# Kernel tuning notes

Measured on AMD Instinct MI355X. Metric: run time of the kernel, lower is better.

## Reference

```python
import jax, jax.numpy as jnp
import numpy as np

N = 100000
E = 1600000
IN_FEATS = 128
OUT_FEATS = 64


def setup_inputs() -> dict:
    key = jax.random.key(0)
    ks = jax.random.split(key, 8)
    node_feat = jax.random.normal(ks[0], (N, IN_FEATS), dtype=jnp.float32)
    edge_feat = jax.random.normal(ks[1], (E, 1), dtype=jnp.float32)
    # Linear params (PyTorch Linear: y = x @ W^T + b; we store W already transposed as [in, out])
    W_node = jax.random.normal(ks[2], (IN_FEATS, OUT_FEATS), dtype=jnp.float32) / np.sqrt(IN_FEATS)
    b_node = jax.random.normal(ks[3], (OUT_FEATS,), dtype=jnp.float32) * 0.01
    W_edge = jax.random.normal(ks[4], (1, OUT_FEATS), dtype=jnp.float32)
    b_edge = jax.random.normal(ks[5], (OUT_FEATS,), dtype=jnp.float32) * 0.01
    src = jax.random.randint(ks[6], (E,), 0, N, dtype=jnp.int32)
    dst = jax.random.randint(ks[7], (E,), 0, N, dtype=jnp.int32)
    return {"node_feat": node_feat, "edge_feat": edge_feat, "W_node": W_node,
            "b_node": b_node, "W_edge": W_edge, "b_edge": b_edge,
            "src": src, "dst": dst}


def reference(node_feat, edge_feat, W_node, b_node, W_edge, b_edge, src, dst):
    n_nodes = node_feat.shape[0]
    # node linear: h = node_fc(node_feat)  -> [N, out]
    h = node_feat @ W_node + b_node
    # edge linear: he = edge_fc(edge_feat) -> [E, out]
    he = edge_feat @ W_edge + b_edge
    # u_add_e: m = h[src] + he  (gather + add)  -> [E, out]
    m = h[src] + he
    # mean aggregate over destination nodes (segment mean; 0 for isolated nodes, as in DGL)
    msg_sum = jax.ops.segment_sum(m, dst, num_segments=n_nodes)  # [N, out]
    deg = jax.ops.segment_sum(jnp.ones((dst.shape[0],), dtype=m.dtype), dst, num_segments=n_nodes)  # [N]
    h_new = msg_sum / jnp.maximum(deg, 1.0)[:, None]
    return h_new
```

## Files before the change

### kernel.cpp

```cpp
#include <hip/hip_runtime.h>

#define IN_F 128
#define OUT_F 64
#define BSH 7
#define BNODES 128
#define NBMAX 800
#define MSC 4096
#define CAPB 4096

typedef __attribute__((ext_vector_type(8))) short short8;
typedef __attribute__((ext_vector_type(4))) float f32x4;

static __device__ __forceinline__ unsigned short f2bf(float f) {
    unsigned u = __float_as_uint(f);
    u += 0x7FFF + ((u >> 16) & 1);
    return (unsigned short)(u >> 16);
}

__global__ void prep(const float* __restrict__ W, unsigned short* __restrict__ Wt,
                     int* __restrict__ gcur, int nb) {
    int i = blockIdx.x * 256 + threadIdx.x;
    if (i < OUT_F * IN_F) {
        int o = i >> 7, k = i & 127;
        Wt[i] = f2bf(W[k * OUT_F + o]);
    }
    if (i < nb) gcur[i] = i * CAPB;
}

__global__ __launch_bounds__(256) void node_linear_mfma(const float* __restrict__ nf,
                                                        const unsigned short* __restrict__ Wt,
                                                        const float* __restrict__ bn,
                                                        unsigned short* __restrict__ h16,
                                                        int n_nodes, int n_tiles) {
    const int lane = threadIdx.x & 63;
    const int wid  = threadIdx.x >> 6;
    const int l15  = lane & 15;
    const int kq   = lane >> 4;

    short8 bfrag[4][4];
#pragma unroll
    for (int c = 0; c < 4; ++c)
#pragma unroll
        for (int ks = 0; ks < 4; ++ks)
            bfrag[c][ks] = *(const short8*)&Wt[(c * 16 + l15) * IN_F + ks * 32 + kq * 8];

    float bv[4];
#pragma unroll
    for (int c = 0; c < 4; ++c) bv[c] = bn[c * 16 + l15];

    for (int tile = blockIdx.x * 4 + wid; tile < n_tiles; tile += gridDim.x * 4) {
        int arow = tile * 16 + l15;
        if (arow >= n_nodes) arow = n_nodes - 1;
        const float* rp = nf + (size_t)arow * IN_F + kq * 8;

        f32x4 acc[4];
#pragma unroll
        for (int c = 0; c < 4; ++c) acc[c] = (f32x4){bv[c], bv[c], bv[c], bv[c]};

#pragma unroll
        for (int ks = 0; ks < 4; ++ks) {
            float4 x0 = *(const float4*)(rp + ks * 32);
            float4 x1 = *(const float4*)(rp + ks * 32 + 4);
            short8 af;
            af[0] = (short)f2bf(x0.x); af[1] = (short)f2bf(x0.y);
            af[2] = (short)f2bf(x0.z); af[3] = (short)f2bf(x0.w);
            af[4] = (short)f2bf(x1.x); af[5] = (short)f2bf(x1.y);
            af[6] = (short)f2bf(x1.z); af[7] = (short)f2bf(x1.w);
#pragma unroll
            for (int c = 0; c < 4; ++c)
                acc[c] = __builtin_amdgcn_mfma_f32_16x16x32_bf16(af, bfrag[c][ks], acc[c], 0, 0, 0);
        }

#pragma unroll
        for (int j = 0; j < 4; ++j) {
            int node = tile * 16 + kq * 4 + j;
            if (node < n_nodes) {
#pragma unroll
                for (int c = 0; c < 4; ++c)
                    h16[(size_t)node * OUT_F + c * 16 + l15] = f2bf(acc[c][j]);
            }
        }
    }
}

__global__ __launch_bounds__(1024) void multisplit(const int* __restrict__ src,
                                                   const int* __restrict__ dst,
                                                   const float* __restrict__ ef,
                                                   int* __restrict__ gcur,
                                                   int2* __restrict__ es,
                                                   int n_edges, int nb) {
    __shared__ int2 stage[MSC];
    __shared__ unsigned short sbuck[MSC];
    __shared__ int lhist[NBMAX];
    __shared__ int lcur[NBMAX];
    __shared__ int gbase[NBMAX];
    __shared__ int wtot[16];

    const int t = threadIdx.x;
    const int cb = blockIdx.x * MSC;
    const int valid = min(MSC, n_edges - cb);
    if (valid <= 0) return;

    for (int i = t; i < nb; i += 1024) lhist[i] = 0;

    int dr[4]; int sr[4]; float fr[4];
#pragma unroll
    for (int k = 0; k < 4; ++k) {
        int i = t + (k << 10);
        if (i < valid) { dr[k] = dst[cb + i]; sr[k] = src[cb + i]; fr[k] = ef[cb + i]; }
        else           { dr[k] = -1; sr[k] = 0; fr[k] = 0.f; }
    }
    __syncthreads();

#pragma unroll
    for (int k = 0; k < 4; ++k)
        if (dr[k] >= 0) atomicAdd(&lhist[dr[k] >> BSH], 1);
    __syncthreads();

    const int wv = t >> 6, lane = t & 63;
    int v = (t < nb) ? lhist[t] : 0;
    int sc = v;
#pragma unroll
    for (int off = 1; off < 64; off <<= 1) {
        int x = __shfl_up(sc, off, 64);
        if (lane >= off) sc += x;
    }
    if (lane == 63) wtot[wv] = sc;
    __syncthreads();
    if (t < 16) {
        int w = wtot[t];
        int s2 = w;
#pragma unroll
        for (int off = 1; off < 16; off <<= 1) {
            int x = __shfl_up(s2, off, 64);
            if (t >= off) s2 += x;
        }
        wtot[t] = s2 - w;
    }
    __syncthreads();
    if (t < nb) lcur[t] = wtot[wv] + (sc - v);
    __syncthreads();

    for (int b = t; b < nb; b += 1024) {
        int c = lhist[b];
        gbase[b] = c ? atomicAdd(&gcur[b], c) : 0;
    }
#pragma unroll
    for (int k = 0; k < 4; ++k) {
        if (dr[k] >= 0) {
            int b = dr[k] >> BSH;
            int p = atomicAdd(&lcur[b], 1);
            int dl = dr[k] & (BNODES - 1);
            stage[p] = make_int2((dl << 17) | sr[k], __float_as_int(fr[k]));
            sbuck[p] = (unsigned short)b;
        }
    }
    __syncthreads();

    for (int i = t; i < valid; i += 1024) {
        int b = sbuck[i];
        int pos = gbase[b] + (i - (lcur[b] - lhist[b]));
        if (pos < (b + 1) * CAPB) es[pos] = stage[i];
    }
}

__global__ __launch_bounds__(512, 8) void aggregate(const unsigned short* __restrict__ h16,
                                                    const int2* __restrict__ es,
                                                    const int* __restrict__ gcur,
                                                    const float* __restrict__ We,
                                                    const float* __restrict__ be,
                                                    float* __restrict__ out, int n_nodes) {
    __shared__ int2 stage[CAPB];
    __shared__ int lhist8[8][BNODES];
    __shared__ int lhist[BNODES];
    __shared__ int lbase[BNODES];
    __shared__ int lcur[BNODES];

    const int t = threadIdx.x;
    const int bkt = blockIdx.x;
    const int s0 = bkt * CAPB;
    int cnt = gcur[bkt] - s0;
    if (cnt > CAPB) cnt = CAPB;

    ((int*)lhist8)[t] = 0;
    ((int*)lhist8)[t + 512] = 0;
    __syncthreads();

    const int wv = t >> 6;
    int2 er[8];
#pragma unroll
    for (int k = 0; k < 8; ++k) {
        int i = t + (k << 9);
        if (i < cnt) er[k] = es[s0 + i];
    }
#pragma unroll
    for (int k = 0; k < 8; ++k) {
        int i = t + (k << 9);
        if (i < cnt) atomicAdd(&lhist8[wv][((unsigned)er[k].x) >> 17], 1);
    }
    __syncthreads();

    if (t < 64) {
        int a = 0, b = 0;
#pragma unroll
        for (int w = 0; w < 8; ++w) { a += lhist8[w][t << 1]; b += lhist8[w][(t << 1) + 1]; }
        lhist[t << 1] = a; lhist[(t << 1) + 1] = b;
        int s = a + b;
#pragma unroll
        for (int off = 1; off < 64; off <<= 1) {
            int x = __shfl_up(s, off, 64);
            if (t >= off) s += x;
        }
        int excl = s - (a + b);
        lbase[t << 1] = excl;       lcur[t << 1] = excl;
        lbase[(t << 1) + 1] = excl + a; lcur[(t << 1) + 1] = excl + a;
    }
    __syncthreads();

#pragma unroll
    for (int k = 0; k < 8; ++k) {
        int i = t + (k << 9);
        if (i < cnt) {
            int b = ((unsigned)er[k].x) >> 17;
            int p = atomicAdd(&lcur[b], 1);
            stage[p] = er[k];
        }
    }
    __syncthreads();

    const int lane = t & 63;
    const int q    = lane >> 4;
    const int o4e  = (lane & 15) << 2;
    const float4 we4 = *(const float4*)&We[o4e];
    const float4 be4 = *(const float4*)&be[o4e];

#pragma unroll
    for (int p = 0; p < 8; ++p) {
        const int dlA = (wv << 4) + (p << 1);
        const int dlB = dlA + 1;
        const int jA = lbase[dlA], dgA = lhist[dlA];
        const int jB = lbase[dlB], dgB = lhist[dlB];
        float4 aA = make_float4(0.f, 0.f, 0.f, 0.f);
        float4 aB = make_float4(0.f, 0.f, 0.f, 0.f);
        float sxA = 0.f, sxB = 0.f;
        const int jm = dgA > dgB ? dgA : dgB;
        for (int j = 0; j < jm; j += 4) {
            int2 eA = make_int2(0, 0), eB = make_int2(0, 0);
            if (j + q < dgA) eA = stage[jA + j + q];
            if (j + q < dgB) eB = stage[jB + j + q];
            uint2 hA = make_uint2(0u, 0u), hB = make_uint2(0u, 0u);
            if (j + q < dgA) hA = *(const uint2*)&h16[((size_t)(eA.x & 0x1FFFF) << 6) + o4e];
            if (j + q < dgB) hB = *(const uint2*)&h16[((size_t)(eB.x & 0x1FFFF) << 6) + o4e];
            aA.x += __uint_as_float(hA.x << 16);
            aA.y += __uint_as_float(hA.x & 0xFFFF0000u);
            aA.z += __uint_as_float(hA.y << 16);
            aA.w += __uint_as_float(hA.y & 0xFFFF0000u);
            sxA  += __int_as_float(eA.y);
            aB.x += __uint_as_float(hB.x << 16);
            aB.y += __uint_as_float(hB.x & 0xFFFF0000u);
            aB.z += __uint_as_float(hB.y << 16);
            aB.w += __uint_as_float(hB.y & 0xFFFF0000u);
            sxB  += __int_as_float(eB.y);
        }
#define RED_(v) { v += __shfl_xor(v, 16, 64); v += __shfl_xor(v, 32, 64); }
        RED_(aA.x) RED_(aA.y) RED_(aA.z) RED_(aA.w) RED_(sxA)
        RED_(aB.x) RED_(aB.y) RED_(aB.z) RED_(aB.w) RED_(sxB)
#undef RED_
        if (q == 0) {
            int nodeA = (bkt << BSH) + dlA;
            if (nodeA < n_nodes) {
                float4 r = make_float4(0.f, 0.f, 0.f, 0.f);
                if (dgA > 0) {
                    float dgf = (float)dgA, inv = 1.f / dgf;
                    r.x = (aA.x + we4.x * sxA + dgf * be4.x) * inv;
                    r.y = (aA.y + we4.y * sxA + dgf * be4.y) * inv;
                    r.z = (aA.z + we4.z * sxA + dgf * be4.z) * inv;
                    r.w = (aA.w + we4.w * sxA + dgf * be4.w) * inv;
                }
                *(float4*)&out[((size_t)nodeA << 6) + o4e] = r;
            }
            int nodeB = (bkt << BSH) + dlB;
            if (nodeB < n_nodes) {
                float4 r = make_float4(0.f, 0.f, 0.f, 0.f);
                if (dgB > 0) {
                    float dgf = (float)dgB, inv = 1.f / dgf;
                    r.x = (aB.x + we4.x * sxB + dgf * be4.x) * inv;
                    r.y = (aB.y + we4.y * sxB + dgf * be4.y) * inv;
                    r.z = (aB.z + we4.z * sxB + dgf * be4.z) * inv;
                    r.w = (aB.w + we4.w * sxB + dgf * be4.w) * inv;
                }
                *(float4*)&out[((size_t)nodeB << 6) + o4e] = r;
            }
        }
    }
}

extern "C" void kernel_launch(void* const* d_in, const int* in_sizes, int n_in,
                              void* d_out, int out_size, void* d_ws, size_t ws_size,
                              hipStream_t stream) {
    const float* nf  = (const float*)d_in[0];
    const float* ef  = (const float*)d_in[1];
    const float* Wn  = (const float*)d_in[2];
    const float* bn  = (const float*)d_in[3];
    const float* We  = (const float*)d_in[4];
    const float* be  = (const float*)d_in[5];
    const int*   src = (const int*)d_in[6];
    const int*   dst = (const int*)d_in[7];
    float* out = (float*)d_out;

    const int n_nodes = in_sizes[0] / IN_F;
    const int n_edges = in_sizes[6];
    const int nb = (n_nodes + BNODES - 1) >> BSH;
    const int n_tiles = (n_nodes + 15) / 16;

    char* w = (char*)d_ws;
    unsigned short* h16 = (unsigned short*)w; w += (size_t)n_nodes * OUT_F * sizeof(unsigned short);
    int2* es  = (int2*)w; w += (size_t)nb * CAPB * sizeof(int2);
    int* gcur = (int*)w;  w += (size_t)NBMAX * sizeof(int);
    unsigned short* Wt = (unsigned short*)w; w += (size_t)OUT_F * IN_F * sizeof(unsigned short);

    prep<<<32, 256, 0, stream>>>(Wn, Wt, gcur, nb);
    node_linear_mfma<<<782, 256, 0, stream>>>(nf, Wt, bn, h16, n_nodes, n_tiles);
    multisplit<<<(n_edges + MSC - 1) / MSC, 1024, 0, stream>>>(src, dst, ef, gcur, es, n_edges, nb);
    aggregate<<<nb, 512, 0, stream>>>(h16, es, gcur, We, be, out, n_nodes);
}
```

Measured before the change: 82.42 us.

## Pack bucket counters, enlarge multisplit chunks, widen aggregate gathers, one tile per wave

The multisplit kernel now handles 6144 edges per block instead of 4096. It packs two bucket cursors into one 32-bit atomic, which halves the global atomics and precomputes the scatter base offsets. Aggregate gathers 16-byte bf16 rows with 8 lanes per edge instead of 8-byte rows with 16 lanes, and relaxes its occupancy hint. The node linear kernel launches one tile per wave instead of grid-striding. Risks are 16-bit counter overflow if a bucket exceeds 65535 edges, higher register pressure, and more LDS per multisplit block.

```diff
diff --git a/kernel.cpp b/kernel.cpp
--- a/kernel.cpp
+++ b/kernel.cpp
@@ -5,7 +5,7 @@
 #define BSH 7
 #define BNODES 128
 #define NBMAX 800
-#define MSC 4096
+#define MSC 6144
 #define CAPB 4096
 
 typedef __attribute__((ext_vector_type(8))) short short8;
@@ -18,13 +18,13 @@
 }
 
 __global__ void prep(const float* __restrict__ W, unsigned short* __restrict__ Wt,
-                     int* __restrict__ gcur, int nb) {
+                     unsigned* __restrict__ gcur2, int npair) {
     int i = blockIdx.x * 256 + threadIdx.x;
     if (i < OUT_F * IN_F) {
         int o = i >> 7, k = i & 127;
         Wt[i] = f2bf(W[k * OUT_F + o]);
     }
-    if (i < nb) gcur[i] = i * CAPB;
+    if (i < npair) gcur2[i] = 0u;
 }
 
 __global__ __launch_bounds__(256) void node_linear_mfma(const float* __restrict__ nf,
@@ -36,6 +36,8 @@
     const int wid  = threadIdx.x >> 6;
     const int l15  = lane & 15;
     const int kq   = lane >> 4;
+    const int tile = blockIdx.x * 4 + wid;
+    if (tile >= n_tiles) return;
 
     short8 bfrag[4][4];
 #pragma unroll
@@ -48,37 +50,35 @@
 #pragma unroll
     for (int c = 0; c < 4; ++c) bv[c] = bn[c * 16 + l15];
 
-    for (int tile = blockIdx.x * 4 + wid; tile < n_tiles; tile += gridDim.x * 4) {
-        int arow = tile * 16 + l15;
-        if (arow >= n_nodes) arow = n_nodes - 1;
-        const float* rp = nf + (size_t)arow * IN_F + kq * 8;
-
-        f32x4 acc[4];
-#pragma unroll
-        for (int c = 0; c < 4; ++c) acc[c] = (f32x4){bv[c], bv[c], bv[c], bv[c]};
-
-#pragma unroll
-        for (int ks = 0; ks < 4; ++ks) {
-            float4 x0 = *(const float4*)(rp + ks * 32);
-            float4 x1 = *(const float4*)(rp + ks * 32 + 4);
-            short8 af;
-            af[0] = (short)f2bf(x0.x); af[1] = (short)f2bf(x0.y);
-            af[2] = (short)f2bf(x0.z); af[3] = (short)f2bf(x0.w);
-            af[4] = (short)f2bf(x1.x); af[5] = (short)f2bf(x1.y);
-            af[6] = (short)f2bf(x1.z); af[7] = (short)f2bf(x1.w);
+    int arow = tile * 16 + l15;
+    if (arow >= n_nodes) arow = n_nodes - 1;
+    const float* rp = nf + (size_t)arow * IN_F + kq * 8;
+
+    f32x4 acc[4];
+#pragma unroll
+    for (int c = 0; c < 4; ++c) acc[c] = (f32x4){bv[c], bv[c], bv[c], bv[c]};
+
+#pragma unroll
+    for (int ks = 0; ks < 4; ++ks) {
+        float4 x0 = *(const float4*)(rp + ks * 32);
+        float4 x1 = *(const float4*)(rp + ks * 32 + 4);
+        short8 af;
+        af[0] = (short)f2bf(x0.x); af[1] = (short)f2bf(x0.y);
+        af[2] = (short)f2bf(x0.z); af[3] = (short)f2bf(x0.w);
+        af[4] = (short)f2bf(x1.x); af[5] = (short)f2bf(x1.y);
+        af[6] = (short)f2bf(x1.z); af[7] = (short)f2bf(x1.w);
+#pragma unroll
+        for (int c = 0; c < 4; ++c)
+            acc[c] = __builtin_amdgcn_mfma_f32_16x16x32_bf16(af, bfrag[c][ks], acc[c], 0, 0, 0);
+    }
+
+#pragma unroll
+    for (int j = 0; j < 4; ++j) {
+        int node = tile * 16 + kq * 4 + j;
+        if (node < n_nodes) {
 #pragma unroll
             for (int c = 0; c < 4; ++c)
-                acc[c] = __builtin_amdgcn_mfma_f32_16x16x32_bf16(af, bfrag[c][ks], acc[c], 0, 0, 0);
-        }
-
-#pragma unroll
-        for (int j = 0; j < 4; ++j) {
-            int node = tile * 16 + kq * 4 + j;
-            if (node < n_nodes) {
-#pragma unroll
-                for (int c = 0; c < 4; ++c)
-                    h16[(size_t)node * OUT_F + c * 16 + l15] = f2bf(acc[c][j]);
-            }
+                h16[(size_t)node * OUT_F + c * 16 + l15] = f2bf(acc[c][j]);
         }
     }
 }
@@ -86,7 +86,7 @@
 __global__ __launch_bounds__(1024) void multisplit(const int* __restrict__ src,
                                                    const int* __restrict__ dst,
                                                    const float* __restrict__ ef,
-                                                   int* __restrict__ gcur,
+                                                   unsigned* __restrict__ gcur2,
                                                    int2* __restrict__ es,
                                                    int n_edges, int nb) {
     __shared__ int2 stage[MSC];
@@ -103,9 +103,9 @@
 
     for (int i = t; i < nb; i += 1024) lhist[i] = 0;
 
-    int dr[4]; int sr[4]; float fr[4];
-#pragma unroll
-    for (int k = 0; k < 4; ++k) {
+    int dr[6]; int sr[6]; float fr[6];
+#pragma unroll
+    for (int k = 0; k < 6; ++k) {
         int i = t + (k << 10);
         if (i < valid) { dr[k] = dst[cb + i]; sr[k] = src[cb + i]; fr[k] = ef[cb + i]; }
         else           { dr[k] = -1; sr[k] = 0; fr[k] = 0.f; }
@@ -113,7 +113,7 @@
     __syncthreads();
 
 #pragma unroll
-    for (int k = 0; k < 4; ++k)
+    for (int k = 0; k < 6; ++k)
         if (dr[k] >= 0) atomicAdd(&lhist[dr[k] >> BSH], 1);
     __syncthreads();
 
@@ -141,12 +141,23 @@
     if (t < nb) lcur[t] = wtot[wv] + (sc - v);
     __syncthreads();
 
-    for (int b = t; b < nb; b += 1024) {
-        int c = lhist[b];
-        gbase[b] = c ? atomicAdd(&gcur[b], c) : 0;
-    }
-#pragma unroll
-    for (int k = 0; k < 4; ++k) {
+    for (int i2 = t; i2 < (nb >> 1); i2 += 1024) {
+        int b0 = i2 << 1;
+        int c0 = lhist[b0], c1 = lhist[b0 + 1];
+        unsigned ret = 0u;
+        if (c0 | c1) ret = atomicAdd(&gcur2[i2], (unsigned)c0 | ((unsigned)c1 << 16));
+        gbase[b0]     = b0 * CAPB + (int)(ret & 0xFFFFu);
+        gbase[b0 + 1] = (b0 + 1) * CAPB + (int)(ret >> 16);
+    }
+    if ((nb & 1) && t == 0) {
+        int b0 = nb - 1;
+        int c0 = lhist[b0];
+        unsigned ret = 0u;
+        if (c0) ret = atomicAdd(&gcur2[nb >> 1], (unsigned)c0);
+        gbase[b0] = b0 * CAPB + (int)(ret & 0xFFFFu);
+    }
+#pragma unroll
+    for (int k = 0; k < 6; ++k) {
         if (dr[k] >= 0) {
             int b = dr[k] >> BSH;
             int p = atomicAdd(&lcur[b], 1);
@@ -157,16 +168,19 @@
     }
     __syncthreads();
 
+    for (int b = t; b < nb; b += 1024) gbase[b] -= (lcur[b] - lhist[b]);
+    __syncthreads();
+
     for (int i = t; i < valid; i += 1024) {
         int b = sbuck[i];
-        int pos = gbase[b] + (i - (lcur[b] - lhist[b]));
+        int pos = gbase[b] + i;
         if (pos < (b + 1) * CAPB) es[pos] = stage[i];
     }
 }
 
-__global__ __launch_bounds__(512, 8) void aggregate(const unsigned short* __restrict__ h16,
+__global__ __launch_bounds__(512, 6) void aggregate(const unsigned short* __restrict__ h16,
                                                     const int2* __restrict__ es,
-                                                    const int* __restrict__ gcur,
+                                                    const unsigned* __restrict__ gcur2,
                                                     const float* __restrict__ We,
                                                     const float* __restrict__ be,
                                                     float* __restrict__ out, int n_nodes) {
@@ -179,7 +193,8 @@
     const int t = threadIdx.x;
     const int bkt = blockIdx.x;
     const int s0 = bkt * CAPB;
-    int cnt = gcur[bkt] - s0;
+    unsigned packed = gcur2[bkt >> 1];
+    int cnt = (bkt & 1) ? (int)(packed >> 16) : (int)(packed & 0xFFFFu);
     if (cnt > CAPB) cnt = CAPB;
 
     ((int*)lhist8)[t] = 0;
@@ -212,7 +227,7 @@
             if (t >= off) s += x;
         }
         int excl = s - (a + b);
-        lbase[t << 1] = excl;       lcur[t << 1] = excl;
+        lbase[t << 1] = excl;           lcur[t << 1] = excl;
         lbase[(t << 1) + 1] = excl + a; lcur[(t << 1) + 1] = excl + a;
     }
     __syncthreads();
@@ -229,67 +244,81 @@
     __syncthreads();
 
     const int lane = t & 63;
-    const int q    = lane >> 4;
-    const int o4e  = (lane & 15) << 2;
-    const float4 we4 = *(const float4*)&We[o4e];
-    const float4 be4 = *(const float4*)&be[o4e];
-
-#pragma unroll
+    const int q    = lane >> 3;
+    const int o8   = (lane & 7) << 3;
+    const float4 weL = *(const float4*)&We[o8];
+    const float4 weH = *(const float4*)&We[o8 + 4];
+    const float4 beL = *(const float4*)&be[o8];
+    const float4 beH = *(const float4*)&be[o8 + 4];
+
     for (int p = 0; p < 8; ++p) {
         const int dlA = (wv << 4) + (p << 1);
         const int dlB = dlA + 1;
         const int jA = lbase[dlA], dgA = lhist[dlA];
         const int jB = lbase[dlB], dgB = lhist[dlB];
-        float4 aA = make_float4(0.f, 0.f, 0.f, 0.f);
-        float4 aB = make_float4(0.f, 0.f, 0.f, 0.f);
+        float aA[8] = {0.f,0.f,0.f,0.f,0.f,0.f,0.f,0.f};
+        float aB[8] = {0.f,0.f,0.f,0.f,0.f,0.f,0.f,0.f};
         float sxA = 0.f, sxB = 0.f;
         const int jm = dgA > dgB ? dgA : dgB;
-        for (int j = 0; j < jm; j += 4) {
+        for (int j = 0; j < jm; j += 8) {
             int2 eA = make_int2(0, 0), eB = make_int2(0, 0);
             if (j + q < dgA) eA = stage[jA + j + q];
             if (j + q < dgB) eB = stage[jB + j + q];
-            uint2 hA = make_uint2(0u, 0u), hB = make_uint2(0u, 0u);
-            if (j + q < dgA) hA = *(const uint2*)&h16[((size_t)(eA.x & 0x1FFFF) << 6) + o4e];
-            if (j + q < dgB) hB = *(const uint2*)&h16[((size_t)(eB.x & 0x1FFFF) << 6) + o4e];
-            aA.x += __uint_as_float(hA.x << 16);
-            aA.y += __uint_as_float(hA.x & 0xFFFF0000u);
-            aA.z += __uint_as_float(hA.y << 16);
-            aA.w += __uint_as_float(hA.y & 0xFFFF0000u);
-            sxA  += __int_as_float(eA.y);
-            aB.x += __uint_as_float(hB.x << 16);
-            aB.y += __uint_as_float(hB.x & 0xFFFF0000u);
-            aB.z += __uint_as_float(hB.y << 16);
-            aB.w += __uint_as_float(hB.y & 0xFFFF0000u);
-            sxB  += __int_as_float(eB.y);
-        }
-#define RED_(v) { v += __shfl_xor(v, 16, 64); v += __shfl_xor(v, 32, 64); }
-        RED_(aA.x) RED_(aA.y) RED_(aA.z) RED_(aA.w) RED_(sxA)
-        RED_(aB.x) RED_(aB.y) RED_(aB.z) RED_(aB.w) RED_(sxB)
+            uint4 hA = make_uint4(0u,0u,0u,0u), hB = make_uint4(0u,0u,0u,0u);
+            if (j + q < dgA) hA = *(const uint4*)&h16[((size_t)(eA.x & 0x1FFFF) << 6) + o8];
+            if (j + q < dgB) hB = *(const uint4*)&h16[((size_t)(eB.x & 0x1FFFF) << 6) + o8];
+            aA[0] += __uint_as_float(hA.x << 16); aA[1] += __uint_as_float(hA.x & 0xFFFF0000u);
+            aA[2] += __uint_as_float(hA.y << 16); aA[3] += __uint_as_float(hA.y & 0xFFFF0000u);
+            aA[4] += __uint_as_float(hA.z << 16); aA[5] += __uint_as_float(hA.z & 0xFFFF0000u);
+            aA[6] += __uint_as_float(hA.w << 16); aA[7] += __uint_as_float(hA.w & 0xFFFF0000u);
+            sxA   += __int_as_float(eA.y);
+            aB[0] += __uint_as_float(hB.x << 16); aB[1] += __uint_as_float(hB.x & 0xFFFF0000u);
+            aB[2] += __uint_as_float(hB.y << 16); aB[3] += __uint_as_float(hB.y & 0xFFFF0000u);
+            aB[4] += __uint_as_float(hB.z << 16); aB[5] += __uint_as_float(hB.z & 0xFFFF0000u);
+            aB[6] += __uint_as_float(hB.w << 16); aB[7] += __uint_as_float(hB.w & 0xFFFF0000u);
+            sxB   += __int_as_float(eB.y);
+        }
+#define RED_(v) { v += __shfl_xor(v, 8, 64); v += __shfl_xor(v, 16, 64); v += __shfl_xor(v, 32, 64); }
+#pragma unroll
+        for (int u = 0; u < 8; ++u) { RED_(aA[u]) }
+#pragma unroll
+        for (int u = 0; u < 8; ++u) { RED_(aB[u]) }
+        RED_(sxA) RED_(sxB)
 #undef RED_
         if (q == 0) {
             int nodeA = (bkt << BSH) + dlA;
             if (nodeA < n_nodes) {
-                float4 r = make_float4(0.f, 0.f, 0.f, 0.f);
+                float4 r0 = make_float4(0.f,0.f,0.f,0.f), r1 = r0;
                 if (dgA > 0) {
                     float dgf = (float)dgA, inv = 1.f / dgf;
-                    r.x = (aA.x + we4.x * sxA + dgf * be4.x) * inv;
-                    r.y = (aA.y + we4.y * sxA + dgf * be4.y) * inv;
-                    r.z = (aA.z + we4.z * sxA + dgf * be4.z) * inv;
-                    r.w = (aA.w + we4.w * sxA + dgf * be4.w) * inv;
+                    r0.x = (aA[0] + weL.x * sxA + dgf * beL.x) * inv;
+                    r0.y = (aA[1] + weL.y * sxA + dgf * beL.y) * inv;
+                    r0.z = (aA[2] + weL.z * sxA + dgf * beL.z) * inv;
+                    r0.w = (aA[3] + weL.w * sxA + dgf * beL.w) * inv;
+                    r1.x = (aA[4] + weH.x * sxA + dgf * beH.x) * inv;
+                    r1.y = (aA[5] + weH.y * sxA + dgf * beH.y) * inv;
+                    r1.z = (aA[6] + weH.z * sxA + dgf * beH.z) * inv;
+                    r1.w = (aA[7] + weH.w * sxA + dgf * beH.w) * inv;
                 }
-                *(float4*)&out[((size_t)nodeA << 6) + o4e] = r;
+                *(float4*)&out[((size_t)nodeA << 6) + o8] = r0;
+                *(float4*)&out[((size_t)nodeA << 6) + o8 + 4] = r1;
             }
             int nodeB = (bkt << BSH) + dlB;
             if (nodeB < n_nodes) {
-                float4 r = make_float4(0.f, 0.f, 0.f, 0.f);
+                float4 r0 = make_float4(0.f,0.f,0.f,0.f), r1 = r0;
                 if (dgB > 0) {
                     float dgf = (float)dgB, inv = 1.f / dgf;
-                    r.x = (aB.x + we4.x * sxB + dgf * be4.x) * inv;
-                    r.y = (aB.y + we4.y * sxB + dgf * be4.y) * inv;
-                    r.z = (aB.z + we4.z * sxB + dgf * be4.z) * inv;
-                    r.w = (aB.w + we4.w * sxB + dgf * be4.w) * inv;
+                    r0.x = (aB[0] + weL.x * sxB + dgf * beL.x) * inv;
+                    r0.y = (aB[1] + weL.y * sxB + dgf * beL.y) * inv;
+                    r0.z = (aB[2] + weL.z * sxB + dgf * beL.z) * inv;
+                    r0.w = (aB[3] + weL.w * sxB + dgf * beL.w) * inv;
+                    r1.x = (aB[4] + weH.x * sxB + dgf * beH.x) * inv;
+                    r1.y = (aB[5] + weH.y * sxB + dgf * beH.y) * inv;
+                    r1.z = (aB[6] + weH.z * sxB + dgf * beH.z) * inv;
+                    r1.w = (aB[7] + weH.w * sxB + dgf * beH.w) * inv;
                 }
-                *(float4*)&out[((size_t)nodeB << 6) + o4e] = r;
+                *(float4*)&out[((size_t)nodeB << 6) + o8] = r0;
+                *(float4*)&out[((size_t)nodeB << 6) + o8 + 4] = r1;
             }
         }
     }
@@ -311,16 +340,17 @@
     const int n_nodes = in_sizes[0] / IN_F;
     const int n_edges = in_sizes[6];
     const int nb = (n_nodes + BNODES - 1) >> BSH;
+    const int npair = (nb + 1) >> 1;
     const int n_tiles = (n_nodes + 15) / 16;
 
     char* w = (char*)d_ws;
     unsigned short* h16 = (unsigned short*)w; w += (size_t)n_nodes * OUT_F * sizeof(unsigned short);
     int2* es  = (int2*)w; w += (size_t)nb * CAPB * sizeof(int2);
-    int* gcur = (int*)w;  w += (size_t)NBMAX * sizeof(int);
+    unsigned* gcur2 = (unsigned*)w; w += 1024 * sizeof(unsigned);
     unsigned short* Wt = (unsigned short*)w; w += (size_t)OUT_F * IN_F * sizeof(unsigned short);
 
-    prep<<<32, 256, 0, stream>>>(Wn, Wt, gcur, nb);
-    node_linear_mfma<<<782, 256, 0, stream>>>(nf, Wt, bn, h16, n_nodes, n_tiles);
-    multisplit<<<(n_edges + MSC - 1) / MSC, 1024, 0, stream>>>(src, dst, ef, gcur, es, n_edges, nb);
-    aggregate<<<nb, 512, 0, stream>>>(h16, es, gcur, We, be, out, n_nodes);
-}
+    prep<<<32, 256, 0, stream>>>(Wn, Wt, gcur2, npair);
+    node_linear_mfma<<<(n_tiles + 3) / 4, 256, 0, stream>>>(nf, Wt, bn, h16, n_nodes, n_tiles);
+    multisplit<<<(n_edges + MSC - 1) / MSC, 1024, 0, stream>>>(src, dst, ef, gcur2, es, n_edges, nb);
+    aggregate<<<nb, 512, 0, stream>>>(h16, es, gcur2, We, be, out, n_nodes);
+}
```

After: 100.5 us. 1.22x slower.
